# Optimization experiments

Measured on AMD Instinct MI355X. Metric: run time of the kernel, lower is better.

The kernel has to match this reference:

```python
import jax, jax.numpy as jnp
import numpy as np

NUM_HEADS = 12

def setup_inputs() -> dict:
    key = jax.random.key(0)
    ks = jax.random.split(key, 5)
    dim = 768
    x = jax.random.normal(ks[0], (2, 64, 64, dim), dtype=jnp.float32)
    qkv_w = jax.random.normal(ks[1], (3 * dim, dim), dtype=jnp.float32) * 0.02
    qkv_b = jax.random.normal(ks[2], (3 * dim,), dtype=jnp.float32) * 0.02
    proj_w = jax.random.normal(ks[3], (dim, dim), dtype=jnp.float32) * 0.02
    proj_b = jax.random.normal(ks[4], (dim,), dtype=jnp.float32) * 0.02
    return {"x": x, "qkv_w": qkv_w, "qkv_b": qkv_b, "proj_w": proj_w, "proj_b": proj_b}

def reference(x, qkv_w, qkv_b, proj_w, proj_b):
    B, H, W, C = x.shape
    N = H * W
    nh = NUM_HEADS
    hd = C // nh
    scale = hd ** -0.5
    # qkv linear: (B,H,W,3C)
    qkv = jnp.einsum('bhwc,dc->bhwd', x, qkv_w) + qkv_b
    qkv = qkv.reshape(B, N, 3, nh, hd).transpose(2, 0, 3, 1, 4)  # (3,B,nh,N,hd)
    q, k, v = qkv[0], qkv[1], qkv[2]
    # (B,nh,N,N) attention scores, stable softmax
    attn = jax.nn.softmax(jnp.einsum('bhqd,bhkd->bhqk', q * scale, k), axis=-1)
    out = jnp.einsum('bhqk,bhkd->bhqd', attn, v)  # (B,nh,N,hd)
    out = out.transpose(0, 2, 1, 3).reshape(B, N, C)
    # Source quirk: for 4D input the output stays (B, N, C) after proj.
    return jnp.einsum('bnc,dc->bnd', out, proj_w) + proj_b
```

## Files before the change

### kernel.cpp

```cpp
#include <hip/hip_runtime.h>
#include <hip/hip_bf16.h>

#define LOG2E 1.44269504088896340736f

typedef __attribute__((ext_vector_type(8))) short short8;
typedef __attribute__((ext_vector_type(4))) float f32x4;
typedef __attribute__((ext_vector_type(16))) float f32x16;

__device__ __forceinline__ unsigned short f2bf(float f) {
    unsigned int u = __float_as_uint(f);
    u += 0x7fffu + ((u >> 16) & 1u);
    return (unsigned short)(u >> 16);
}

__device__ __forceinline__ unsigned cvt_pk_bf16(float a, float b) {
    unsigned r;
    asm("v_cvt_pk_bf16_f32 %0, %1, %2" : "=v"(r) : "v"(a), "v"(b));
    return r;
}

__device__ __forceinline__ float fast_exp2(float x) {
    float r;
    asm("v_exp_f32 %0, %1" : "=v"(r) : "v"(x));
    return r;
}

__global__ void cvt_f32_to_bf16(const float* __restrict__ in,
                                unsigned short* __restrict__ out, int n4) {
    int stride = gridDim.x * blockDim.x;
    for (int i = blockIdx.x * blockDim.x + threadIdx.x; i < n4; i += stride) {
        float4 v = ((const float4*)in)[i];
        ushort4 o;
        o.x = f2bf(v.x); o.y = f2bf(v.y); o.z = f2bf(v.z); o.w = f2bf(v.w);
        ((ushort4*)out)[i] = o;
    }
}

template <int EPI>
__global__ __launch_bounds__(256, 2)
void gemm_bt(const unsigned short* __restrict__ A,
             const unsigned short* __restrict__ B,
             const float* __restrict__ bias,
             void* __restrict__ Cout,
             int M, int N, int K) {
    __shared__ unsigned short As[128][72];
    __shared__ unsigned short Bs[128][72];

    const int tid  = threadIdx.x;
    const int wave = tid >> 6, lane = tid & 63;
    const int fr = lane & 15, fg = lane >> 4;
    const int wm = (wave >> 1) * 64, wn = (wave & 1) * 64;
    const int m0 = blockIdx.y * 128, n0 = blockIdx.x * 128;
    const int trow = tid >> 3, tseg = tid & 7;

    f32x4 acc[4][4];
#pragma unroll
    for (int m = 0; m < 4; m++)
#pragma unroll
        for (int n = 0; n < 4; n++) acc[m][n] = (f32x4){0.f, 0.f, 0.f, 0.f};

    short8 rA[4], rB[4];
#pragma unroll
    for (int c = 0; c < 4; c++) {
        int r = trow + c * 32;
        rA[c] = *(const short8*)(A + (size_t)(m0 + r) * K + tseg * 8);
        rB[c] = *(const short8*)(B + (size_t)(n0 + r) * K + tseg * 8);
    }

    for (int k0 = 0; k0 < K; k0 += 64) {
        __syncthreads();
#pragma unroll
        for (int c = 0; c < 4; c++) {
            int r = trow + c * 32;
            *(short8*)&As[r][tseg * 8] = rA[c];
            *(short8*)&Bs[r][tseg * 8] = rB[c];
        }
        if (k0 + 64 < K) {
#pragma unroll
            for (int c = 0; c < 4; c++) {
                int r = trow + c * 32;
                rA[c] = *(const short8*)(A + (size_t)(m0 + r) * K + k0 + 64 + tseg * 8);
                rB[c] = *(const short8*)(B + (size_t)(n0 + r) * K + k0 + 64 + tseg * 8);
            }
        }
        __syncthreads();
#pragma unroll
        for (int ks = 0; ks < 2; ks++) {
            short8 af[4], bfr[4];
#pragma unroll
            for (int m = 0; m < 4; m++)
                af[m] = *(const short8*)&As[wm + m * 16 + fr][ks * 32 + fg * 8];
#pragma unroll
            for (int n = 0; n < 4; n++)
                bfr[n] = *(const short8*)&Bs[wn + n * 16 + fr][ks * 32 + fg * 8];
#pragma unroll
            for (int m = 0; m < 4; m++)
#pragma unroll
                for (int n = 0; n < 4; n++)
                    acc[m][n] = __builtin_amdgcn_mfma_f32_16x16x32_bf16(
                        af[m], bfr[n], acc[m][n], 0, 0, 0);
        }
    }

#pragma unroll
    for (int m = 0; m < 4; m++) {
#pragma unroll
        for (int n = 0; n < 4; n++) {
            int gn = n0 + wn + n * 16 + fr;
            float bv = bias[gn];
#pragma unroll
            for (int j = 0; j < 4; j++) {
                int gm = m0 + wm + m * 16 + fg * 4 + j;
                float v = acc[m][n][j] + bv;
                if (EPI == 0) {
                    int which = gn / 768, rem = gn % 768;
                    int h = rem >> 6, d = rem & 63;
                    int b = gm >> 12, nn = gm & 4095;
                    if (which == 0) v *= (0.125f * LOG2E);
                    unsigned short* o = (unsigned short*)Cout;
                    size_t base = (((size_t)which * 2 + b) * 12 + h) * 262144;
                    if (which == 2)
                        o[base + (size_t)d * 4096 + nn] = f2bf(v);
                    else
                        o[base + (size_t)nn * 64 + d] = f2bf(v);
                } else {
                    float* o = (float*)Cout;
                    o[(size_t)gm * 768 + gn] = v;
                }
            }
        }
    }
}

__global__ __launch_bounds__(256, 2)
void attn_fwd(const unsigned short* __restrict__ qkv,
              unsigned short* __restrict__ outp) {
    __shared__ unsigned short Ks[64][72];
    __shared__ unsigned short Vt[64][72];

    const int tid  = threadIdx.x;
    const int wave = tid >> 6, lane = tid & 63;
    const int l31 = lane & 31, hh = lane >> 5;
    const int l31p = (l31 & 0x13) | ((l31 & 4) << 1) | ((l31 & 8) >> 1);

    const int qt = blockIdx.x;
    const int bh = blockIdx.y;
    const int b = bh / 12, h = bh % 12;

    const size_t headsz = (size_t)4096 * 64;
    const unsigned short* qh  = qkv + ((size_t)b * 12 + h) * headsz;
    const unsigned short* kh  = qkv + ((size_t)(2 + b) * 12 + h) * headsz;
    const unsigned short* vht = qkv + ((size_t)(4 + b) * 12 + h) * headsz;

    const int qw = qt * 128 + wave * 32;
    const int gq = qw + l31;

    short8 qf[4];
#pragma unroll
    for (int ks = 0; ks < 4; ks++)
        qf[ks] = *(const short8*)(qh + (size_t)gq * 64 + ks * 16 + hh * 8);

    float mrow = -1e30f, lrow = 0.f;
    f32x16 accA = (f32x16)0.f, accB = (f32x16)0.f;

    const int r = tid >> 3, sg = tid & 7;

    short8 rK[2], rV[2];
#pragma unroll
    for (int c = 0; c < 2; c++) {
        int kr = r + c * 32;
        rK[c] = *(const short8*)(kh + (size_t)kr * 64 + sg * 8);
        rV[c] = *(const short8*)(vht + (size_t)kr * 4096 + sg * 8);
    }

    for (int kt = 0; kt < 64; kt++) {
        __syncthreads();
#pragma unroll
        for (int c = 0; c < 2; c++) {
            int kr = r + c * 32;
            *(short8*)&Ks[kr][sg * 8] = rK[c];
            *(short8*)&Vt[kr][sg * 8] = rV[c];
        }
        if (kt < 63) {
            const unsigned short* kb = kh + (size_t)(kt + 1) * 4096;
#pragma unroll
            for (int c = 0; c < 2; c++) {
                int kr = r + c * 32;
                rK[c] = *(const short8*)(kb + kr * 64 + sg * 8);
                rV[c] = *(const short8*)(vht + (size_t)kr * 4096 + (kt + 1) * 64 + sg * 8);
            }
        }
        __syncthreads();

        f32x16 s0 = (f32x16)0.f, s1 = (f32x16)0.f;
        __builtin_amdgcn_s_setprio(1);
#pragma unroll
        for (int ks = 0; ks < 4; ks++) {
            short8 kf0 = *(const short8*)&Ks[l31p][ks * 16 + hh * 8];
            short8 kf1 = *(const short8*)&Ks[32 + l31p][ks * 16 + hh * 8];
            s0 = __builtin_amdgcn_mfma_f32_32x32x16_bf16(kf0, qf[ks], s0, 0, 0, 0);
            s1 = __builtin_amdgcn_mfma_f32_32x32x16_bf16(kf1, qf[ks], s1, 0, 0, 0);
        }
        __builtin_amdgcn_s_setprio(0);

        float t[16];
#pragma unroll
        for (int i = 0; i < 8; i++) t[i] = fmaxf(s0[2 * i], s0[2 * i + 1]);
#pragma unroll
        for (int i = 0; i < 8; i++) t[i + 8] = fmaxf(s1[2 * i], s1[2 * i + 1]);
#pragma unroll
        for (int w = 8; w; w >>= 1)
#pragma unroll
            for (int i = 0; i < 8; i++)
                if (i < w) t[i] = fmaxf(t[i], t[i + w]);
        float mx = fmaxf(t[0], __shfl_xor(t[0], 32));

        if (!__all(mx - mrow <= 8.0f)) {
            float mnew = fmaxf(mrow, mx);
            float corr = fast_exp2(mrow - mnew);
            mrow = mnew;
            lrow *= corr;
#pragma unroll
            for (int i = 0; i < 16; i++) { accA[i] *= corr; accB[i] *= corr; }
        }
#pragma unroll
        for (int i = 0; i < 16; i++) {
            s0[i] = fast_exp2(s0[i] - mrow);
            s1[i] = fast_exp2(s1[i] - mrow);
        }
#pragma unroll
        for (int i = 0; i < 8; i++) t[i] = s0[2 * i] + s0[2 * i + 1];
#pragma unroll
        for (int i = 0; i < 8; i++) t[i + 8] = s1[2 * i] + s1[2 * i + 1];
#pragma unroll
        for (int w = 8; w; w >>= 1)
#pragma unroll
            for (int i = 0; i < 8; i++)
                if (i < w) t[i] += t[i + w];
        lrow += t[0] + __shfl_xor(t[0], 32);

        short8 pf[4];
        {
            union { unsigned w[4]; short8 v; } up;
            up.w[0] = cvt_pk_bf16(s0[0], s0[1]);  up.w[1] = cvt_pk_bf16(s0[2], s0[3]);
            up.w[2] = cvt_pk_bf16(s0[4], s0[5]);  up.w[3] = cvt_pk_bf16(s0[6], s0[7]);
            pf[0] = up.v;
            up.w[0] = cvt_pk_bf16(s0[8], s0[9]);  up.w[1] = cvt_pk_bf16(s0[10], s0[11]);
            up.w[2] = cvt_pk_bf16(s0[12], s0[13]); up.w[3] = cvt_pk_bf16(s0[14], s0[15]);
            pf[1] = up.v;
            up.w[0] = cvt_pk_bf16(s1[0], s1[1]);  up.w[1] = cvt_pk_bf16(s1[2], s1[3]);
            up.w[2] = cvt_pk_bf16(s1[4], s1[5]);  up.w[3] = cvt_pk_bf16(s1[6], s1[7]);
            pf[2] = up.v;
            up.w[0] = cvt_pk_bf16(s1[8], s1[9]);  up.w[1] = cvt_pk_bf16(s1[10], s1[11]);
            up.w[2] = cvt_pk_bf16(s1[12], s1[13]); up.w[3] = cvt_pk_bf16(s1[14], s1[15]);
            pf[3] = up.v;
        }

        __builtin_amdgcn_s_setprio(1);
#pragma unroll
        for (int ks2 = 0; ks2 < 4; ks2++) {
            short8 vf0 = *(const short8*)&Vt[l31][ks2 * 16 + hh * 8];
            short8 vf1 = *(const short8*)&Vt[32 + l31][ks2 * 16 + hh * 8];
            accA = __builtin_amdgcn_mfma_f32_32x32x16_bf16(vf0, pf[ks2], accA, 0, 0, 0);
            accB = __builtin_amdgcn_mfma_f32_32x32x16_bf16(vf1, pf[ks2], accB, 0, 0, 0);
        }
        __builtin_amdgcn_s_setprio(0);
    }

    float inv = 1.0f / lrow;
    size_t rowoff = (size_t)(b * 4096 + gq) * 768 + h * 64;
#pragma unroll
    for (int g = 0; g < 4; g++) {
        ushort4 o;
        o.x = f2bf(accA[4 * g + 0] * inv);
        o.y = f2bf(accA[4 * g + 1] * inv);
        o.z = f2bf(accA[4 * g + 2] * inv);
        o.w = f2bf(accA[4 * g + 3] * inv);
        *(ushort4*)(outp + rowoff + g * 8 + hh * 4) = o;
        o.x = f2bf(accB[4 * g + 0] * inv);
        o.y = f2bf(accB[4 * g + 1] * inv);
        o.z = f2bf(accB[4 * g + 2] * inv);
        o.w = f2bf(accB[4 * g + 3] * inv);
        *(ushort4*)(outp + rowoff + 32 + g * 8 + hh * 4) = o;
    }
}

extern "C" void kernel_launch(void* const* d_in, const int* in_sizes, int n_in,
                              void* d_out, int out_size, void* d_ws, size_t ws_size,
                              hipStream_t stream) {
    const float* x      = (const float*)d_in[0];
    const float* qkv_w  = (const float*)d_in[1];
    const float* qkv_b  = (const float*)d_in[2];
    const float* proj_w = (const float*)d_in[3];
    const float* proj_b = (const float*)d_in[4];
    float* out = (float*)d_out;

    char* ws = (char*)d_ws;
    unsigned short* x_bf    = (unsigned short*)(ws);
    unsigned short* w1_bf   = (unsigned short*)(ws + 12582912);
    unsigned short* w2_bf   = (unsigned short*)(ws + 16121856);
    unsigned short* qkv_sep = (unsigned short*)(ws + 17301504);
    unsigned short* att     = (unsigned short*)(ws + 55050240);

    cvt_f32_to_bf16<<<2048, 256, 0, stream>>>(x,      x_bf,  6291456 / 4);
    cvt_f32_to_bf16<<<1024, 256, 0, stream>>>(qkv_w,  w1_bf, 1769472 / 4);
    cvt_f32_to_bf16<<<576,  256, 0, stream>>>(proj_w, w2_bf,  589824 / 4);

    gemm_bt<0><<<dim3(18, 64), 256, 0, stream>>>(x_bf, w1_bf, qkv_b, qkv_sep,
                                                 8192, 2304, 768);

    attn_fwd<<<dim3(32, 24), 256, 0, stream>>>(qkv_sep, att);

    gemm_bt<1><<<dim3(6, 64), 256, 0, stream>>>(att, w2_bf, proj_b, out,
                                                8192, 768, 768);
}
```

Measured before the change: 226.3 us.

## Use direct global-to-LDS loads with XOR-swizzled layouts and double buffering

Both the GEMM and attention kernels now load tiles straight into shared memory with global_load_lds into double-buffered, unpadded tiles, which removes the register staging path and one barrier per iteration. Data is pre-swizzled in global memory by the conversion kernel and the QKV/attention epilogues, so the LDS reads that feed the MFMA fragments avoid bank conflicts. Attention also keeps its row-sum in per-lane packed partials that are reduced only once at the end, and raises its occupancy hint to 3. The change couples layouts across kernels, so any mismatch in the swizzle conventions would silently corrupt results.

```diff
diff --git a/kernel.cpp b/kernel.cpp
--- a/kernel.cpp
+++ b/kernel.cpp
@@ -4,6 +4,7 @@
 #define LOG2E 1.44269504088896340736f
 
 typedef __attribute__((ext_vector_type(8))) short short8;
+typedef __attribute__((ext_vector_type(2))) float f32x2;
 typedef __attribute__((ext_vector_type(4))) float f32x4;
 typedef __attribute__((ext_vector_type(16))) float f32x16;
 
@@ -25,14 +26,28 @@
     return r;
 }
 
-__global__ void cvt_f32_to_bf16(const float* __restrict__ in,
-                                unsigned short* __restrict__ out, int n4) {
+__device__ __forceinline__ void gl_lds16(const unsigned short* g, unsigned short* l) {
+    __builtin_amdgcn_global_load_lds(
+        (const __attribute__((address_space(1))) unsigned int*)g,
+        (__attribute__((address_space(3))) unsigned int*)l, 16, 0, 0);
+}
+
+__global__ void cvt_swz(const float* __restrict__ in,
+                        unsigned short* __restrict__ out, int n8) {
     int stride = gridDim.x * blockDim.x;
-    for (int i = blockIdx.x * blockDim.x + threadIdx.x; i < n4; i += stride) {
-        float4 v = ((const float4*)in)[i];
-        ushort4 o;
-        o.x = f2bf(v.x); o.y = f2bf(v.y); o.z = f2bf(v.z); o.w = f2bf(v.w);
-        ((ushort4*)out)[i] = o;
+    for (int i = blockIdx.x * blockDim.x + threadIdx.x; i < n8; i += stride) {
+        int flat = i * 8;
+        int row = flat / 768;
+        int col = flat - row * 768;
+        float4 v0 = ((const float4*)(in + flat))[0];
+        float4 v1 = ((const float4*)(in + flat))[1];
+        union { unsigned short u[8]; short8 v; } o;
+        o.u[0] = f2bf(v0.x); o.u[1] = f2bf(v0.y);
+        o.u[2] = f2bf(v0.z); o.u[3] = f2bf(v0.w);
+        o.u[4] = f2bf(v1.x); o.u[5] = f2bf(v1.y);
+        o.u[6] = f2bf(v1.z); o.u[7] = f2bf(v1.w);
+        int c = (col & 63) ^ ((row & 7) << 3);
+        *(short8*)(out + (size_t)row * 768 + (col & ~63) + c) = o.v;
     }
 }
 
@@ -43,15 +58,15 @@
              const float* __restrict__ bias,
              void* __restrict__ Cout,
              int M, int N, int K) {
-    __shared__ unsigned short As[128][72];
-    __shared__ unsigned short Bs[128][72];
+    __shared__ unsigned short As[2][8192];
+    __shared__ unsigned short Bs[2][8192];
 
     const int tid  = threadIdx.x;
     const int wave = tid >> 6, lane = tid & 63;
     const int fr = lane & 15, fg = lane >> 4;
     const int wm = (wave >> 1) * 64, wn = (wave & 1) * 64;
     const int m0 = blockIdx.y * 128, n0 = blockIdx.x * 128;
-    const int trow = tid >> 3, tseg = tid & 7;
+    const int sr = lane >> 3, ss = lane & 7;
 
     f32x4 acc[4][4];
 #pragma unroll
@@ -59,40 +74,39 @@
 #pragma unroll
         for (int n = 0; n < 4; n++) acc[m][n] = (f32x4){0.f, 0.f, 0.f, 0.f};
 
-    short8 rA[4], rB[4];
-#pragma unroll
-    for (int c = 0; c < 4; c++) {
-        int r = trow + c * 32;
-        rA[c] = *(const short8*)(A + (size_t)(m0 + r) * K + tseg * 8);
-        rB[c] = *(const short8*)(B + (size_t)(n0 + r) * K + tseg * 8);
-    }
-
-    for (int k0 = 0; k0 < K; k0 += 64) {
+    const int NT = K >> 6;
+
+#define GEMM_STAGE(buf, k0)                                                     \
+    {                                                                           \
+        _Pragma("unroll")                                                       \
+        for (int c = 0; c < 4; c++) {                                           \
+            int rr = (c * 4 + wave) * 8 + sr;                                   \
+            gl_lds16(A + (size_t)(m0 + rr) * K + (k0) + ss * 8,                 \
+                     &As[buf][(c * 4 + wave) * 512]);                           \
+            gl_lds16(B + (size_t)(n0 + rr) * K + (k0) + ss * 8,                 \
+                     &Bs[buf][(c * 4 + wave) * 512]);                           \
+        }                                                                       \
+    }
+
+    GEMM_STAGE(0, 0)
+
+    for (int t = 0; t < NT; t++) {
         __syncthreads();
-#pragma unroll
-        for (int c = 0; c < 4; c++) {
-            int r = trow + c * 32;
-            *(short8*)&As[r][tseg * 8] = rA[c];
-            *(short8*)&Bs[r][tseg * 8] = rB[c];
-        }
-        if (k0 + 64 < K) {
-#pragma unroll
-            for (int c = 0; c < 4; c++) {
-                int r = trow + c * 32;
-                rA[c] = *(const short8*)(A + (size_t)(m0 + r) * K + k0 + 64 + tseg * 8);
-                rB[c] = *(const short8*)(B + (size_t)(n0 + r) * K + k0 + 64 + tseg * 8);
-            }
-        }
-        __syncthreads();
+        if (t + 1 < NT) GEMM_STAGE((t + 1) & 1, (t + 1) << 6)
+        const unsigned short* ab = As[t & 1];
+        const unsigned short* bb = Bs[t & 1];
+        __builtin_amdgcn_s_setprio(1);
 #pragma unroll
         for (int ks = 0; ks < 2; ks++) {
             short8 af[4], bfr[4];
 #pragma unroll
             for (int m = 0; m < 4; m++)
-                af[m] = *(const short8*)&As[wm + m * 16 + fr][ks * 32 + fg * 8];
+                af[m] = *(const short8*)&ab[(wm + m * 16 + fr) * 64 +
+                                            (((ks * 4 + fg) ^ (fr & 7)) << 3)];
 #pragma unroll
             for (int n = 0; n < 4; n++)
-                bfr[n] = *(const short8*)&Bs[wn + n * 16 + fr][ks * 32 + fg * 8];
+                bfr[n] = *(const short8*)&bb[(wn + n * 16 + fr) * 64 +
+                                             (((ks * 4 + fg) ^ (fr & 7)) << 3)];
 #pragma unroll
             for (int m = 0; m < 4; m++)
 #pragma unroll
@@ -100,7 +114,9 @@
                     acc[m][n] = __builtin_amdgcn_mfma_f32_16x16x32_bf16(
                         af[m], bfr[n], acc[m][n], 0, 0, 0);
         }
-    }
+        __builtin_amdgcn_s_setprio(0);
+    }
+#undef GEMM_STAGE
 
 #pragma unroll
     for (int m = 0; m < 4; m++) {
@@ -119,10 +135,17 @@
                     if (which == 0) v *= (0.125f * LOG2E);
                     unsigned short* o = (unsigned short*)Cout;
                     size_t base = (((size_t)which * 2 + b) * 12 + h) * 262144;
-                    if (which == 2)
-                        o[base + (size_t)d * 4096 + nn] = f2bf(v);
-                    else
+                    if (which == 2) {
+                        int c = nn & 63;
+                        int cc = (c & 7) | (((c >> 3) ^ (d & 7)) << 3);
+                        o[base + (size_t)d * 4096 + (nn & ~63) + cc] = f2bf(v);
+                    } else if (which == 1) {
+                        int sk = (nn & 3) | ((nn & 8) >> 1);
+                        int dd = (d & 7) | (((d >> 3) ^ sk) << 3);
+                        o[base + (size_t)nn * 64 + dd] = f2bf(v);
+                    } else {
                         o[base + (size_t)nn * 64 + d] = f2bf(v);
+                    }
                 } else {
                     float* o = (float*)Cout;
                     o[(size_t)gm * 768 + gn] = v;
@@ -132,16 +155,18 @@
     }
 }
 
-__global__ __launch_bounds__(256, 2)
+__global__ __launch_bounds__(256, 3)
 void attn_fwd(const unsigned short* __restrict__ qkv,
               unsigned short* __restrict__ outp) {
-    __shared__ unsigned short Ks[64][72];
-    __shared__ unsigned short Vt[64][72];
+    __shared__ unsigned short KsF[2][4096];
+    __shared__ unsigned short VtF[2][4096];
 
     const int tid  = threadIdx.x;
     const int wave = tid >> 6, lane = tid & 63;
     const int l31 = lane & 31, hh = lane >> 5;
     const int l31p = (l31 & 0x13) | ((l31 & 4) << 1) | ((l31 & 8) >> 1);
+    const int sKp  = (l31p & 3) | ((l31p & 8) >> 1);
+    const int sV   = l31 & 7;
 
     const int qt = blockIdx.x;
     const int bh = blockIdx.y;
@@ -160,115 +185,126 @@
     for (int ks = 0; ks < 4; ks++)
         qf[ks] = *(const short8*)(qh + (size_t)gq * 64 + ks * 16 + hh * 8);
 
-    float mrow = -1e30f, lrow = 0.f;
+    float mrow = -1e30f;
     f32x16 accA = (f32x16)0.f, accB = (f32x16)0.f;
-
-    const int r = tid >> 3, sg = tid & 7;
-
-    short8 rK[2], rV[2];
-#pragma unroll
-    for (int c = 0; c < 2; c++) {
-        int kr = r + c * 32;
-        rK[c] = *(const short8*)(kh + (size_t)kr * 64 + sg * 8);
-        rV[c] = *(const short8*)(vht + (size_t)kr * 4096 + sg * 8);
-    }
+    f32x2 ls[16];
+#pragma unroll
+    for (int i = 0; i < 16; i++) ls[i] = (f32x2){0.f, 0.f};
+
+    const int sr = lane >> 3, ss = lane & 7;
+
+#define ATTN_STAGE(buf, kt)                                                     \
+    {                                                                           \
+        _Pragma("unroll")                                                       \
+        for (int c = 0; c < 2; c++) {                                           \
+            int rr = (c * 4 + wave) * 8 + sr;                                   \
+            gl_lds16(kh + (size_t)(kt) * 4096 + rr * 64 + ss * 8,               \
+                     &KsF[buf][(c * 4 + wave) * 512]);                          \
+            gl_lds16(vht + (size_t)rr * 4096 + (kt) * 64 + ss * 8,              \
+                     &VtF[buf][(c * 4 + wave) * 512]);                          \
+        }                                                                       \
+    }
+
+    ATTN_STAGE(0, 0)
 
     for (int kt = 0; kt < 64; kt++) {
         __syncthreads();
-#pragma unroll
-        for (int c = 0; c < 2; c++) {
-            int kr = r + c * 32;
-            *(short8*)&Ks[kr][sg * 8] = rK[c];
-            *(short8*)&Vt[kr][sg * 8] = rV[c];
-        }
-        if (kt < 63) {
-            const unsigned short* kb = kh + (size_t)(kt + 1) * 4096;
-#pragma unroll
-            for (int c = 0; c < 2; c++) {
-                int kr = r + c * 32;
-                rK[c] = *(const short8*)(kb + kr * 64 + sg * 8);
-                rV[c] = *(const short8*)(vht + (size_t)kr * 4096 + (kt + 1) * 64 + sg * 8);
-            }
-        }
-        __syncthreads();
+        if (kt < 63) ATTN_STAGE((kt + 1) & 1, kt + 1)
+        const unsigned short* ks_ = KsF[kt & 1];
+        const unsigned short* vt_ = VtF[kt & 1];
 
         f32x16 s0 = (f32x16)0.f, s1 = (f32x16)0.f;
         __builtin_amdgcn_s_setprio(1);
 #pragma unroll
         for (int ks = 0; ks < 4; ks++) {
-            short8 kf0 = *(const short8*)&Ks[l31p][ks * 16 + hh * 8];
-            short8 kf1 = *(const short8*)&Ks[32 + l31p][ks * 16 + hh * 8];
+            short8 kf0 = *(const short8*)&ks_[l31p * 64 +
+                                              (((ks * 2 + hh) ^ sKp) << 3)];
+            short8 kf1 = *(const short8*)&ks_[(32 + l31p) * 64 +
+                                              (((ks * 2 + hh) ^ sKp) << 3)];
             s0 = __builtin_amdgcn_mfma_f32_32x32x16_bf16(kf0, qf[ks], s0, 0, 0, 0);
             s1 = __builtin_amdgcn_mfma_f32_32x32x16_bf16(kf1, qf[ks], s1, 0, 0, 0);
         }
         __builtin_amdgcn_s_setprio(0);
 
-        float t[16];
-#pragma unroll
-        for (int i = 0; i < 8; i++) t[i] = fmaxf(s0[2 * i], s0[2 * i + 1]);
-#pragma unroll
-        for (int i = 0; i < 8; i++) t[i + 8] = fmaxf(s1[2 * i], s1[2 * i + 1]);
-#pragma unroll
-        for (int w = 8; w; w >>= 1)
-#pragma unroll
-            for (int i = 0; i < 8; i++)
-                if (i < w) t[i] = fmaxf(t[i], t[i + w]);
-        float mx = fmaxf(t[0], __shfl_xor(t[0], 32));
+        union F16 { f32x16 v; f32x2 p[8]; float f[16]; };
+        F16 a, b2;
+        a.v = s0; b2.v = s1;
+
+        f32x2 m2[8];
+#pragma unroll
+        for (int i = 0; i < 8; i++) m2[i] = __builtin_elementwise_max(a.p[i], b2.p[i]);
+#pragma unroll
+        for (int i = 0; i < 4; i++) m2[i] = __builtin_elementwise_max(m2[i], m2[i + 4]);
+        m2[0] = __builtin_elementwise_max(m2[0], m2[2]);
+        m2[1] = __builtin_elementwise_max(m2[1], m2[3]);
+        m2[0] = __builtin_elementwise_max(m2[0], m2[1]);
+        float mx = fmaxf(m2[0][0], m2[0][1]);
+        mx = fmaxf(mx, __shfl_xor(mx, 32));
 
         if (!__all(mx - mrow <= 8.0f)) {
             float mnew = fmaxf(mrow, mx);
             float corr = fast_exp2(mrow - mnew);
             mrow = mnew;
-            lrow *= corr;
+            f32x2 c2 = {corr, corr};
 #pragma unroll
             for (int i = 0; i < 16; i++) { accA[i] *= corr; accB[i] *= corr; }
-        }
+#pragma unroll
+            for (int i = 0; i < 16; i++) ls[i] *= c2;
+        }
+
+        f32x2 nm = {-mrow, -mrow};
+#pragma unroll
+        for (int i = 0; i < 8; i++) { a.p[i] += nm; b2.p[i] += nm; }
 #pragma unroll
         for (int i = 0; i < 16; i++) {
-            s0[i] = fast_exp2(s0[i] - mrow);
-            s1[i] = fast_exp2(s1[i] - mrow);
-        }
-#pragma unroll
-        for (int i = 0; i < 8; i++) t[i] = s0[2 * i] + s0[2 * i + 1];
-#pragma unroll
-        for (int i = 0; i < 8; i++) t[i + 8] = s1[2 * i] + s1[2 * i + 1];
-#pragma unroll
-        for (int w = 8; w; w >>= 1)
-#pragma unroll
-            for (int i = 0; i < 8; i++)
-                if (i < w) t[i] += t[i + w];
-        lrow += t[0] + __shfl_xor(t[0], 32);
+            a.f[i]  = fast_exp2(a.f[i]);
+            b2.f[i] = fast_exp2(b2.f[i]);
+        }
+#pragma unroll
+        for (int i = 0; i < 8; i++) { ls[i] += a.p[i]; ls[8 + i] += b2.p[i]; }
 
         short8 pf[4];
         {
             union { unsigned w[4]; short8 v; } up;
-            up.w[0] = cvt_pk_bf16(s0[0], s0[1]);  up.w[1] = cvt_pk_bf16(s0[2], s0[3]);
-            up.w[2] = cvt_pk_bf16(s0[4], s0[5]);  up.w[3] = cvt_pk_bf16(s0[6], s0[7]);
+            up.w[0] = cvt_pk_bf16(a.f[0], a.f[1]);   up.w[1] = cvt_pk_bf16(a.f[2], a.f[3]);
+            up.w[2] = cvt_pk_bf16(a.f[4], a.f[5]);   up.w[3] = cvt_pk_bf16(a.f[6], a.f[7]);
             pf[0] = up.v;
-            up.w[0] = cvt_pk_bf16(s0[8], s0[9]);  up.w[1] = cvt_pk_bf16(s0[10], s0[11]);
-            up.w[2] = cvt_pk_bf16(s0[12], s0[13]); up.w[3] = cvt_pk_bf16(s0[14], s0[15]);
+            up.w[0] = cvt_pk_bf16(a.f[8], a.f[9]);   up.w[1] = cvt_pk_bf16(a.f[10], a.f[11]);
+            up.w[2] = cvt_pk_bf16(a.f[12], a.f[13]); up.w[3] = cvt_pk_bf16(a.f[14], a.f[15]);
             pf[1] = up.v;
-            up.w[0] = cvt_pk_bf16(s1[0], s1[1]);  up.w[1] = cvt_pk_bf16(s1[2], s1[3]);
-            up.w[2] = cvt_pk_bf16(s1[4], s1[5]);  up.w[3] = cvt_pk_bf16(s1[6], s1[7]);
+            up.w[0] = cvt_pk_bf16(b2.f[0], b2.f[1]);   up.w[1] = cvt_pk_bf16(b2.f[2], b2.f[3]);
+            up.w[2] = cvt_pk_bf16(b2.f[4], b2.f[5]);   up.w[3] = cvt_pk_bf16(b2.f[6], b2.f[7]);
             pf[2] = up.v;
-            up.w[0] = cvt_pk_bf16(s1[8], s1[9]);  up.w[1] = cvt_pk_bf16(s1[10], s1[11]);
-            up.w[2] = cvt_pk_bf16(s1[12], s1[13]); up.w[3] = cvt_pk_bf16(s1[14], s1[15]);
+            up.w[0] = cvt_pk_bf16(b2.f[8], b2.f[9]);   up.w[1] = cvt_pk_bf16(b2.f[10], b2.f[11]);
+            up.w[2] = cvt_pk_bf16(b2.f[12], b2.f[13]); up.w[3] = cvt_pk_bf16(b2.f[14], b2.f[15]);
             pf[3] = up.v;
         }
 
         __builtin_amdgcn_s_setprio(1);
 #pragma unroll
         for (int ks2 = 0; ks2 < 4; ks2++) {
-            short8 vf0 = *(const short8*)&Vt[l31][ks2 * 16 + hh * 8];
-            short8 vf1 = *(const short8*)&Vt[32 + l31][ks2 * 16 + hh * 8];
+            short8 vf0 = *(const short8*)&vt_[l31 * 64 +
+                                              (((ks2 * 2 + hh) ^ sV) << 3)];
+            short8 vf1 = *(const short8*)&vt_[(32 + l31) * 64 +
+                                              (((ks2 * 2 + hh) ^ sV) << 3)];
             accA = __builtin_amdgcn_mfma_f32_32x32x16_bf16(vf0, pf[ks2], accA, 0, 0, 0);
             accB = __builtin_amdgcn_mfma_f32_32x32x16_bf16(vf1, pf[ks2], accB, 0, 0, 0);
         }
         __builtin_amdgcn_s_setprio(0);
     }
-
-    float inv = 1.0f / lrow;
+#undef ATTN_STAGE
+
+#pragma unroll
+    for (int w = 8; w >= 1; w >>= 1)
+#pragma unroll
+        for (int i = 0; i < 8; i++)
+            if (i < w) ls[i] += ls[i + w];
+    float lr = ls[0][0] + ls[0][1];
+    lr += __shfl_xor(lr, 32);
+    float inv = 1.0f / lr;
+
     size_t rowoff = (size_t)(b * 4096 + gq) * 768 + h * 64;
+    int sw = l31 & 7;
 #pragma unroll
     for (int g = 0; g < 4; g++) {
         ushort4 o;
@@ -276,12 +312,12 @@
         o.y = f2bf(accA[4 * g + 1] * inv);
         o.z = f2bf(accA[4 * g + 2] * inv);
         o.w = f2bf(accA[4 * g + 3] * inv);
-        *(ushort4*)(outp + rowoff + g * 8 + hh * 4) = o;
+        *(ushort4*)(outp + rowoff + ((g ^ sw) * 8) + hh * 4) = o;
         o.x = f2bf(accB[4 * g + 0] * inv);
         o.y = f2bf(accB[4 * g + 1] * inv);
         o.z = f2bf(accB[4 * g + 2] * inv);
         o.w = f2bf(accB[4 * g + 3] * inv);
-        *(ushort4*)(outp + rowoff + 32 + g * 8 + hh * 4) = o;
+        *(ushort4*)(outp + rowoff + (((4 + g) ^ sw) * 8) + hh * 4) = o;
     }
 }
 
@@ -302,9 +338,9 @@
     unsigned short* qkv_sep = (unsigned short*)(ws + 17301504);
     unsigned short* att     = (unsigned short*)(ws + 55050240);
 
-    cvt_f32_to_bf16<<<2048, 256, 0, stream>>>(x,      x_bf,  6291456 / 4);
-    cvt_f32_to_bf16<<<1024, 256, 0, stream>>>(qkv_w,  w1_bf, 1769472 / 4);
-    cvt_f32_to_bf16<<<576,  256, 0, stream>>>(proj_w, w2_bf,  589824 / 4);
+    cvt_swz<<<2048, 256, 0, stream>>>(x,      x_bf,  6291456 / 8);
+    cvt_swz<<<864,  256, 0, stream>>>(qkv_w,  w1_bf, 1769472 / 8);
+    cvt_swz<<<288,  256, 0, stream>>>(proj_w, w2_bf,  589824 / 8);
 
     gemm_bt<0><<<dim3(18, 64), 256, 0, stream>>>(x_bf, w1_bf, qkv_b, qkv_sep,
                                                  8192, 2304, 768);
```

After: 229.3 us. Within noise of the previous version (+1.3%).
